# Optimization experiments

Hardware: AMD Instinct MI355X
Metric: run time of the kernel (lower is better)

Reference implementation:

```python
import jax, jax.numpy as jnp
import numpy as np

N, E, E3, DIM = 25000, 50000, 40000, 64


def setup_inputs() -> dict:
    key = jax.random.key(0)
    ks = jax.random.split(key, 16)
    def g(k, shape, scale=0.1):
        return jax.random.normal(k, shape, jnp.float32) * scale
    return {
        "x": jax.random.normal(ks[0], (N, 8), jnp.float32),
        "edge_attr": jax.random.uniform(ks[1], (E, 19), dtype=jnp.float32),
        "edge_attr3": jax.random.uniform(ks[2], (E3, 8), dtype=jnp.float32),
        "edge_index": jax.random.randint(ks[3], (2, E), 0, N),
        "edge_index3": jax.random.randint(ks[4], (2, E3), 0, N),
        "W_node": g(ks[5], (8, DIM)), "b_node": jnp.zeros((DIM,), jnp.float32),
        "W_ea": g(ks[6], (19, 12)), "b_ea": jnp.zeros((12,), jnp.float32),
        "W_e1": g(ks[7], (12, 128)), "b_e1": jnp.zeros((128,), jnp.float32),
        "W_e2": g(ks[8], (128, DIM * DIM), 0.01), "b_e2": jnp.zeros((DIM * DIM,), jnp.float32),
        "conv_bias": jnp.zeros((DIM,), jnp.float32),
        "W_ih": g(ks[9], (3 * DIM, DIM)), "b_ih": jnp.zeros((3 * DIM,), jnp.float32),
        "W_hh": g(ks[10], (3 * DIM, DIM)), "b_hh": jnp.zeros((3 * DIM,), jnp.float32),
        "W_l1": g(ks[11], (DIM + 8, 128)), "b_l1": jnp.zeros((128,), jnp.float32),
        "W_l2": g(ks[12], (128, 1)), "b_l2": jnp.zeros((1,), jnp.float32),
    }


def _forward(x, edge_attr, edge_attr3,
             W_node, b_node, W_ea, b_ea, W_e1, b_e1, W_e2, b_e2, conv_bias,
             W_ih, b_ih, W_hh, b_hh, W_l1, b_l1, W_l2, b_l2,
             edge_index, edge_index3):
    dim = W_node.shape[1]
    n = x.shape[0]
    out = jax.nn.relu(x @ W_node + b_node)                      # [N, dim]
    ea = jax.nn.relu(edge_attr @ W_ea + b_ea)                   # [E, 12]
    # edge MLP -> per-edge dim x dim weight matrices (same for all 3 conv calls)
    Wedge = (jax.nn.relu(ea @ W_e1 + b_e1) @ W_e2 + b_e2).reshape(-1, dim, dim)  # [E, dim, dim]
    src, dst = edge_index[0], edge_index[1]
    ones = jnp.ones((src.shape[0],), x.dtype)
    cnt = jnp.maximum(jax.ops.segment_sum(ones, dst, num_segments=n), 1.0)  # [N]
    h = out
    for _ in range(3):
        msg = jnp.einsum('ed,edf->ef', out[src], Wedge)                     # per-edge GEMV
        agg = jax.ops.segment_sum(msg, dst, num_segments=n) / cnt[:, None]  # scatter-mean
        m = jax.nn.relu(agg + conv_bias)
        # single-step GRU (PyTorch gate order: r, z, n)
        gi = m @ W_ih.T + b_ih
        gh = h @ W_hh.T + b_hh
        ir, iz, inn = jnp.split(gi, 3, axis=-1)
        hr, hz, hn = jnp.split(gh, 3, axis=-1)
        r = jax.nn.sigmoid(ir + hr)
        z = jax.nn.sigmoid(iz + hz)
        ng = jnp.tanh(inn + r * hn)
        h = (1.0 - z) * ng + z * h
        out = h
    pair = (out[edge_index3[0]] + out[edge_index3[1]]) * 0.5    # mean over the 2 endpoints
    yhat = jnp.concatenate([pair, edge_attr3], axis=1)          # [E3, dim+8]
    yhat = jax.nn.relu(yhat @ W_l1 + b_l1) @ W_l2 + b_l2        # [E3, 1]
    return yhat[:, 0]


def reference(x, edge_attr, edge_attr3, edge_index, edge_index3,
              W_node, b_node, W_ea, b_ea, W_e1, b_e1, W_e2, b_e2, conv_bias,
              W_ih, b_ih, W_hh, b_hh, W_l1, b_l1, W_l2, b_l2):
    return _forward(x, edge_attr, edge_attr3,
                    W_node, b_node, W_ea, b_ea, W_e1, b_e1, W_e2, b_e2, conv_bias,
                    W_ih, b_ih, W_hh, b_hh, W_l1, b_l1, W_l2, b_l2,
                    edge_index, edge_index3)
```

## Files before the change

kernel.cpp:

```cpp
#include <hip/hip_runtime.h>

typedef unsigned short u16;
typedef unsigned int u32;
typedef __attribute__((ext_vector_type(8))) short short8v;
typedef __attribute__((ext_vector_type(4))) float float4v;

__device__ __forceinline__ float sigm(float x) { return 1.0f / (1.0f + __expf(-x)); }
__device__ __forceinline__ u16 f2bf(float f) {
  u32 u = __float_as_uint(f);
  u32 r = (u + 0x7fffu + ((u >> 16) & 1u)) >> 16;
  return (u16)r;
}
__device__ __forceinline__ float bf2f(u16 w) { return __uint_as_float(((u32)w) << 16); }

__global__ void k_zero_f(float* __restrict__ p, int n) {
  int i = blockIdx.x * blockDim.x + threadIdx.x;
  if (i < n) p[i] = 0.0f;
}
__global__ void k_zero_i(int* __restrict__ p, int n) {
  int i = blockIdx.x * blockDim.x + threadIdx.x;
  if (i < n) p[i] = 0;
}

__global__ void k_cnt(const int* __restrict__ dst, int* __restrict__ cnt, int E) {
  int e = blockIdx.x * blockDim.x + threadIdx.x;
  if (e < E) atomicAdd(&cnt[dst[e]], 1);
}

__global__ void k_node(const float* __restrict__ x, const float* __restrict__ Wn,
                       const float* __restrict__ bn, float* __restrict__ h, int N) {
  int tid = blockIdx.x * blockDim.x + threadIdx.x;
  if (tid >= N * 64) return;
  int n = tid >> 6, f = tid & 63;
  float acc = bn[f];
  for (int k = 0; k < 8; ++k) acc += x[(size_t)n * 8 + k] * Wn[k * 64 + f];
  h[tid] = fmaxf(acc, 0.0f);
}

__global__ __launch_bounds__(256) void k_edge_mlp(
    const float* __restrict__ ea_in, const float* __restrict__ Wea,
    const float* __restrict__ bea, const float* __restrict__ We1,
    const float* __restrict__ be1, u16* __restrict__ Ahi, int E) {
  __shared__ float att[2][19];
  __shared__ float ea[2][12];
  int half = threadIdx.x >> 7;
  int t = threadIdx.x & 127;
  int e = blockIdx.x * 2 + half;
  bool real = (e < E);
  int ee = real ? e : E - 1;
  if (t < 19) att[half][t] = ea_in[(size_t)ee * 19 + t];
  __syncthreads();
  if (t < 12) {
    float a = bea[t];
#pragma unroll
    for (int k = 0; k < 19; ++k) a += att[half][k] * Wea[k * 12 + t];
    ea[half][t] = fmaxf(a, 0.0f);
  }
  __syncthreads();
  float a = be1[t];
#pragma unroll
  for (int j = 0; j < 12; ++j) a += ea[half][j] * We1[j * 128 + t];
  if (real) Ahi[(size_t)e * 128 + t] = f2bf(fmaxf(a, 0.0f));
}

__global__ void k_pack_b(const float* __restrict__ W2, u16* __restrict__ Bph) {
  int tid = blockIdx.x * blockDim.x + threadIdx.x;
  if (tid >= 128 * 4096) return;
  int j = tid & 7;
  int lane = (tid >> 3) & 63;
  int nt = (tid >> 9) & 3;
  int ks = (tid >> 11) & 3;
  int d = tid >> 13;
  int c = lane & 15, q = lane >> 4;
  int k = ks * 32 + q * 8 + j;
  int n = d * 64 + nt * 16 + c;
  Bph[tid] = f2bf(W2[(size_t)k * 4096 + n]);
}

__global__ void k_prep_wtf(const float* __restrict__ Wih, const float* __restrict__ Whh,
                           u16* __restrict__ WpI, u16* __restrict__ WpH) {
  int tid = blockIdx.x * blockDim.x + threadIdx.x;
  if (tid >= 2 * 12288) return;
  int w = tid / 12288;
  int r = tid - w * 12288;
  int jj = r & 7;
  int lane = (r >> 3) & 63;
  int t = r >> 9;
  int nt = t % 12, ks = t / 12;
  int c = lane & 15, q = lane >> 4;
  int j = nt * 16 + c;
  int k = ks * 32 + q * 8 + jj;
  const float* W = w ? Whh : Wih;
  u16* Wp = w ? WpH : WpI;
  Wp[r] = f2bf(W[j * 64 + k]);
}

__global__ void k_prep_wl1(const float* __restrict__ Wl1, u16* __restrict__ Wp1) {
  int tid = blockIdx.x * blockDim.x + threadIdx.x;
  if (tid >= 3 * 8 * 64 * 8) return;
  int j = tid & 7;
  int lane = (tid >> 3) & 63;
  int nt = (tid >> 9) & 7;
  int ks = tid >> 12;
  int c = lane & 15, q = lane >> 4;
  int k = ks * 32 + q * 8 + j;
  int n = nt * 16 + c;
  Wp1[tid] = f2bf((k < 72) ? Wl1[k * 128 + n] : 0.0f);
}

__global__ __launch_bounds__(256, 2) void k_conv_fused(
    const u16* __restrict__ Ahi, const u16* __restrict__ Bph,
    const float* __restrict__ b2, const float* __restrict__ h,
    const int* __restrict__ src, const int* __restrict__ dst,
    float* __restrict__ agg, int E) {
  __shared__ __align__(16) u16 sAh[128 * 136];
  __shared__ __align__(16) float hs[128 * 36];
  __shared__ __align__(16) float sb2[2048];
  int m0 = blockIdx.x * 128;
  int d0 = blockIdx.y * 32;
  int tid = threadIdx.x;
#pragma unroll
  for (int p = 0; p < 8; ++p) {
    int slot = p * 256 + tid;
    int r = slot >> 4, s = slot & 15;
    int gr = m0 + r;
    if (gr >= E) gr = E - 1;
    *(uint4*)(&sAh[r * 136 + s * 8]) = *(const uint4*)(Ahi + (size_t)gr * 128 + s * 8);
  }
#pragma unroll
  for (int p = 0; p < 4; ++p) {
    int slot = p * 256 + tid;
    int r = slot >> 3, s = slot & 7;
    int ge = m0 + r;
    if (ge >= E) ge = E - 1;
    int sn = src[ge];
    *(float4*)(&hs[r * 36 + s * 4]) = *(const float4*)(h + (size_t)sn * 64 + d0 + s * 4);
  }
#pragma unroll
  for (int p = 0; p < 2; ++p) {
    int slot = p * 256 + tid;
    *(float4*)(&sb2[slot * 4]) = *(const float4*)(b2 + d0 * 64 + slot * 4);
  }
  __syncthreads();
  int wave = tid >> 6, lane = tid & 63;
  int c = lane & 15, q = lane >> 4;
  float msg[2][4][4];
#pragma unroll
  for (int mt = 0; mt < 2; ++mt)
#pragma unroll
    for (int nt = 0; nt < 4; ++nt)
#pragma unroll
      for (int r = 0; r < 4; ++r) msg[mt][nt][r] = 0.0f;

  short8v bufA[16], bufB[16];
  auto loadB = [&](int dd, short8v* buf) {
    const u16* bp = Bph + (size_t)dd * 8192 + lane * 8;
#pragma unroll
    for (int i = 0; i < 16; ++i) buf[i] = *(const short8v*)(bp + i * 512);
  };
  auto compute = [&](int dd, const short8v* buf) {
    int dl = dd - d0;
#pragma unroll
    for (int mt = 0; mt < 2; ++mt) {
      int arow = wave * 32 + mt * 16 + c;
      float4v acc[4];
#pragma unroll
      for (int nt = 0; nt < 4; ++nt) acc[nt] = (float4v){0.f, 0.f, 0.f, 0.f};
#pragma unroll
      for (int ks = 0; ks < 4; ++ks) {
        short8v ah = *(const short8v*)(&sAh[arow * 136 + ks * 32 + q * 8]);
#pragma unroll
        for (int nt = 0; nt < 4; ++nt)
          acc[nt] = __builtin_amdgcn_mfma_f32_16x16x32_bf16(ah, buf[ks * 4 + nt], acc[nt], 0, 0, 0);
      }
      float hd[4];
#pragma unroll
      for (int r = 0; r < 4; ++r)
        hd[r] = hs[(wave * 32 + mt * 16 + q * 4 + r) * 36 + dl];
#pragma unroll
      for (int nt = 0; nt < 4; ++nt) {
        float b2v = sb2[dl * 64 + nt * 16 + c];
#pragma unroll
        for (int r = 0; r < 4; ++r) msg[mt][nt][r] += hd[r] * (acc[nt][r] + b2v);
      }
    }
  };

  loadB(d0, bufA);
  for (int d = d0; d < d0 + 32; d += 2) {
    loadB(d + 1, bufB);
    compute(d, bufA);
    if (d + 2 < d0 + 32) loadB(d + 2, bufA);
    compute(d + 1, bufB);
  }
#pragma unroll
  for (int mt = 0; mt < 2; ++mt) {
#pragma unroll
    for (int r = 0; r < 4; ++r) {
      int e = m0 + wave * 32 + mt * 16 + q * 4 + r;
      if (e < E) {
        int dn = dst[e];
        float* ap = agg + (size_t)dn * 64 + c;
#pragma unroll
        for (int nt = 0; nt < 4; ++nt) atomicAdd(ap + nt * 16, msg[mt][nt][r]);
      }
    }
  }
}

__global__ __launch_bounds__(256, 2) void k_gru_mfma(
    float* __restrict__ agg, const int* __restrict__ cnt,
    const float* __restrict__ cb, const u16* __restrict__ WpI,
    const u16* __restrict__ WpH, const float* __restrict__ bih,
    const float* __restrict__ bhh, const float* __restrict__ hin,
    float* __restrict__ hout, int N) {
  __shared__ __align__(16) u16 sM[64 * 72];
  __shared__ __align__(16) u16 sH[64 * 72];
  __shared__ __align__(16) float sHf[64 * 68];
  int n0 = blockIdx.x * 64;
  int tid = threadIdx.x;
#pragma unroll
  for (int p = 0; p < 16; ++p) {
    int slot = p * 256 + tid;
    int n = slot >> 6, f = slot & 63;
    int gn = n0 + n;
    bool real = (gn < N);
    if (!real) gn = N - 1;
    float cf = fmaxf((float)cnt[gn], 1.0f);
    float av = agg[(size_t)gn * 64 + f];
    if (real) agg[(size_t)gn * 64 + f] = 0.0f;
    float m = fmaxf(av / cf + cb[f], 0.0f);
    float hv = hin[(size_t)gn * 64 + f];
    sM[n * 72 + f] = f2bf(m);
    sH[n * 72 + f] = f2bf(hv);
    sHf[n * 68 + f] = hv;
  }
  __syncthreads();
  int wave = tid >> 6, lane = tid & 63;
  int c = lane & 15, q = lane >> 4;
  short8v am[2], ah[2];
#pragma unroll
  for (int ks = 0; ks < 2; ++ks) {
    am[ks] = *(const short8v*)(&sM[(wave * 16 + c) * 72 + ks * 32 + q * 8]);
    ah[ks] = *(const short8v*)(&sH[(wave * 16 + c) * 72 + ks * 32 + q * 8]);
  }
  float4v accRZ[8], accN[4], accHN[4];
#pragma unroll
  for (int i = 0; i < 8; ++i) accRZ[i] = (float4v){0.f, 0.f, 0.f, 0.f};
#pragma unroll
  for (int i = 0; i < 4; ++i) {
    accN[i] = (float4v){0.f, 0.f, 0.f, 0.f};
    accHN[i] = (float4v){0.f, 0.f, 0.f, 0.f};
  }
#pragma unroll
  for (int ks = 0; ks < 2; ++ks) {
#pragma unroll
    for (int nt = 0; nt < 8; ++nt) {
      short8v bI = *(const short8v*)(WpI + ((size_t)(ks * 12 + nt) * 64 + lane) * 8);
      short8v bH = *(const short8v*)(WpH + ((size_t)(ks * 12 + nt) * 64 + lane) * 8);
      accRZ[nt] = __builtin_amdgcn_mfma_f32_16x16x32_bf16(am[ks], bI, accRZ[nt], 0, 0, 0);
      accRZ[nt] = __builtin_amdgcn_mfma_f32_16x16x32_bf16(ah[ks], bH, accRZ[nt], 0, 0, 0);
    }
#pragma unroll
    for (int nt = 0; nt < 4; ++nt) {
      short8v bI = *(const short8v*)(WpI + ((size_t)(ks * 12 + 8 + nt) * 64 + lane) * 8);
      short8v bH = *(const short8v*)(WpH + ((size_t)(ks * 12 + 8 + nt) * 64 + lane) * 8);
      accN[nt] = __builtin_amdgcn_mfma_f32_16x16x32_bf16(am[ks], bI, accN[nt], 0, 0, 0);
      accHN[nt] = __builtin_amdgcn_mfma_f32_16x16x32_bf16(ah[ks], bH, accHN[nt], 0, 0, 0);
    }
  }
#pragma unroll
  for (int nt = 0; nt < 4; ++nt) {
    int f = nt * 16 + c;
    float brz_r = bih[f] + bhh[f];
    float brz_z = bih[64 + f] + bhh[64 + f];
    float bin = bih[128 + f];
    float bhn = bhh[128 + f];
#pragma unroll
    for (int r = 0; r < 4; ++r) {
      int nl = wave * 16 + q * 4 + r;
      int gn = n0 + nl;
      float rr = sigm(accRZ[nt][r] + brz_r);
      float zz = sigm(accRZ[nt + 4][r] + brz_z);
      float ng = tanhf(accN[nt][r] + bin + rr * (accHN[nt][r] + bhn));
      float hv = sHf[nl * 68 + f];
      if (gn < N) hout[(size_t)gn * 64 + f] = (1.0f - zz) * ng + zz * hv;
    }
  }
}

__global__ __launch_bounds__(256) void k_final_mfma(
    const float* __restrict__ h, const float* __restrict__ ea3,
    const int* __restrict__ idx3, const u16* __restrict__ Wp1,
    const float* __restrict__ bl1, const float* __restrict__ Wl2,
    const float* __restrict__ bl2, float* __restrict__ out, int E3) {
  __shared__ __align__(16) u16 sF[64 * 104];
  int e0 = blockIdx.x * 64;
  int tid = threadIdx.x;
  {
    int er = tid >> 2;
    int part = tid & 3;
    int ge = e0 + er;
    int gc = (ge < E3) ? ge : E3 - 1;
    int a = idx3[gc], b = idx3[E3 + gc];
    for (int kk = part * 24; kk < part * 24 + 24; ++kk) {
      float v;
      if (kk < 64) v = 0.5f * (h[(size_t)a * 64 + kk] + h[(size_t)b * 64 + kk]);
      else if (kk < 72) v = ea3[(size_t)gc * 8 + (kk - 64)];
      else v = 0.0f;
      sF[er * 104 + kk] = f2bf(v);
    }
  }
  __syncthreads();
  int wave = tid >> 6, lane = tid & 63;
  int c = lane & 15, q = lane >> 4;
  float4v acc[8];
#pragma unroll
  for (int nt = 0; nt < 8; ++nt) acc[nt] = (float4v){0.f, 0.f, 0.f, 0.f};
#pragma unroll
  for (int ks = 0; ks < 3; ++ks) {
    short8v af = *(const short8v*)(&sF[(wave * 16 + c) * 104 + ks * 32 + q * 8]);
#pragma unroll
    for (int nt = 0; nt < 8; ++nt) {
      short8v bf = *(const short8v*)(Wp1 + ((size_t)(ks * 8 + nt) * 64 + lane) * 8);
      acc[nt] = __builtin_amdgcn_mfma_f32_16x16x32_bf16(af, bf, acc[nt], 0, 0, 0);
    }
  }
  float v[4] = {0.f, 0.f, 0.f, 0.f};
#pragma unroll
  for (int nt = 0; nt < 8; ++nt) {
    int n = nt * 16 + c;
    float b1 = bl1[n];
    float w2 = Wl2[n];
#pragma unroll
    for (int r = 0; r < 4; ++r) v[r] += fmaxf(acc[nt][r] + b1, 0.0f) * w2;
  }
#pragma unroll
  for (int off = 1; off < 16; off <<= 1) {
#pragma unroll
    for (int r = 0; r < 4; ++r) v[r] += __shfl_xor(v[r], off);
  }
  if (c == 0) {
    float b2v = bl2[0];
#pragma unroll
    for (int r = 0; r < 4; ++r) {
      int e = e0 + wave * 16 + q * 4 + r;
      if (e < E3) out[e] = v[r] + b2v;
    }
  }
}

extern "C" void kernel_launch(void* const* d_in, const int* in_sizes, int n_in,
                              void* d_out, int out_size, void* d_ws, size_t ws_size,
                              hipStream_t stream) {
  const float* x          = (const float*)d_in[0];
  const float* edge_attr  = (const float*)d_in[1];
  const float* edge_attr3 = (const float*)d_in[2];
  const int*   edge_index = (const int*)d_in[3];
  const int*   edge_index3= (const int*)d_in[4];
  const float* W_node = (const float*)d_in[5];
  const float* b_node = (const float*)d_in[6];
  const float* W_ea   = (const float*)d_in[7];
  const float* b_ea   = (const float*)d_in[8];
  const float* W_e1   = (const float*)d_in[9];
  const float* b_e1   = (const float*)d_in[10];
  const float* W_e2   = (const float*)d_in[11];
  const float* b_e2   = (const float*)d_in[12];
  const float* conv_bias = (const float*)d_in[13];
  const float* W_ih   = (const float*)d_in[14];
  const float* b_ih   = (const float*)d_in[15];
  const float* W_hh   = (const float*)d_in[16];
  const float* b_hh   = (const float*)d_in[17];
  const float* W_l1   = (const float*)d_in[18];
  const float* b_l1   = (const float*)d_in[19];
  const float* W_l2   = (const float*)d_in[20];
  const float* b_l2   = (const float*)d_in[21];

  int N  = in_sizes[0] / 8;
  int E  = in_sizes[1] / 19;
  int E3 = in_sizes[2] / 8;

  char* p = (char*)d_ws;
  auto carve = [&](size_t bytes) -> void* {
    char* q = p;
    p += (bytes + 255) & ~(size_t)255;
    return (void*)q;
  };
  float* hA   = (float*)carve((size_t)N * 64 * 4);
  float* hB   = (float*)carve((size_t)N * 64 * 4);
  float* agg  = (float*)carve((size_t)N * 64 * 4);
  int*   cnt  = (int*)carve((size_t)N * 4);
  u16*   Ahi  = (u16*)carve((size_t)E * 128 * 2);
  u16*   Bph  = (u16*)carve((size_t)128 * 4096 * 2);
  u16*   WpI  = (u16*)carve(12288 * 2);
  u16*   WpH  = (u16*)carve(12288 * 2);
  u16*   Wp1  = (u16*)carve(12288 * 2);

  const int* src = edge_index;
  const int* dst = edge_index + E;

  k_zero_i<<<(N + 255) / 256, 256, 0, stream>>>(cnt, N);
  k_cnt<<<(E + 255) / 256, 256, 0, stream>>>(dst, cnt, E);
  k_node<<<((size_t)N * 64 + 255) / 256, 256, 0, stream>>>(x, W_node, b_node, hA, N);
  k_edge_mlp<<<(E + 1) / 2, 256, 0, stream>>>(edge_attr, W_ea, b_ea, W_e1, b_e1, Ahi, E);
  k_pack_b<<<(128 * 4096 + 255) / 256, 256, 0, stream>>>(W_e2, Bph);
  k_prep_wtf<<<(2 * 12288 + 255) / 256, 256, 0, stream>>>(W_ih, W_hh, WpI, WpH);
  k_prep_wl1<<<(12288 + 255) / 256, 256, 0, stream>>>(W_l1, Wp1);
  k_zero_f<<<((size_t)N * 64 + 255) / 256, 256, 0, stream>>>(agg, N * 64);

  float* hcur = hA;
  float* hnxt = hB;
  dim3 gconv((E + 127) / 128, 2);
  int ngru = (N + 63) / 64;
  for (int it = 0; it < 3; ++it) {
    k_conv_fused<<<gconv, 256, 0, stream>>>(Ahi, Bph, b_e2, hcur, src, dst, agg, E);
    k_gru_mfma<<<ngru, 256, 0, stream>>>(agg, cnt, conv_bias, WpI, WpH,
                                         b_ih, b_hh, hcur, hnxt, N);
    float* tmp = hcur; hcur = hnxt; hnxt = tmp;
  }
  k_final_mfma<<<(E3 + 63) / 64, 256, 0, stream>>>(hcur, edge_attr3, edge_index3, Wp1,
                                                   b_l1, W_l2, b_l2, (float*)d_out, E3);
}
```

Before: 448.7 us.

## Stage edge-MLP weights in LDS via async loads and keep A fragments in registers

```diff
diff --git a/kernel.cpp b/kernel.cpp
--- a/kernel.cpp
+++ b/kernel.cpp
@@ -113,20 +113,38 @@
     const float* __restrict__ b2, const float* __restrict__ h,
     const int* __restrict__ src, const int* __restrict__ dst,
     float* __restrict__ agg, int E) {
-  __shared__ __align__(16) u16 sAh[128 * 136];
+  __shared__ __align__(16) u16 sB[2][8192];
   __shared__ __align__(16) float hs[128 * 36];
   __shared__ __align__(16) float sb2[2048];
   int m0 = blockIdx.x * 128;
   int d0 = blockIdx.y * 32;
   int tid = threadIdx.x;
-#pragma unroll
-  for (int p = 0; p < 8; ++p) {
-    int slot = p * 256 + tid;
-    int r = slot >> 4, s = slot & 15;
-    int gr = m0 + r;
+  int wave = tid >> 6, lane = tid & 63;
+  int mw = wave >> 1, fw = wave & 1;
+  int c = lane & 15, q = lane >> 4;
+
+  auto stageB = [&](int d, int b) {
+    const u16* gp = Bph + (size_t)d * 8192 + wave * 2048 + lane * 8;
+    u16* lp = &sB[b][wave * 2048];
+#pragma unroll
+    for (int i = 0; i < 4; ++i)
+      __builtin_amdgcn_global_load_lds(
+          (const __attribute__((address_space(1))) unsigned int*)(gp + i * 512),
+          (__attribute__((address_space(3))) unsigned int*)(lp + i * 512), 16, 0, 0);
+  };
+
+  stageB(d0, 0);
+
+  short8v afr[4][4];
+#pragma unroll
+  for (int mt = 0; mt < 4; ++mt) {
+    int gr = m0 + mw * 64 + mt * 16 + c;
     if (gr >= E) gr = E - 1;
-    *(uint4*)(&sAh[r * 136 + s * 8]) = *(const uint4*)(Ahi + (size_t)gr * 128 + s * 8);
-  }
+    const u16* ap = Ahi + (size_t)gr * 128 + q * 8;
+#pragma unroll
+    for (int ks = 0; ks < 4; ++ks) afr[mt][ks] = *(const short8v*)(ap + ks * 32);
+  }
+
 #pragma unroll
   for (int p = 0; p < 4; ++p) {
     int slot = p * 256 + tid;
@@ -142,67 +160,60 @@
     *(float4*)(&sb2[slot * 4]) = *(const float4*)(b2 + d0 * 64 + slot * 4);
   }
   __syncthreads();
-  int wave = tid >> 6, lane = tid & 63;
-  int c = lane & 15, q = lane >> 4;
-  float msg[2][4][4];
-#pragma unroll
-  for (int mt = 0; mt < 2; ++mt)
-#pragma unroll
-    for (int nt = 0; nt < 4; ++nt)
+
+  float msg[4][2][4];
+#pragma unroll
+  for (int mt = 0; mt < 4; ++mt)
+#pragma unroll
+    for (int nt = 0; nt < 2; ++nt)
 #pragma unroll
       for (int r = 0; r < 4; ++r) msg[mt][nt][r] = 0.0f;
 
-  short8v bufA[16], bufB[16];
-  auto loadB = [&](int dd, short8v* buf) {
-    const u16* bp = Bph + (size_t)dd * 8192 + lane * 8;
-#pragma unroll
-    for (int i = 0; i < 16; ++i) buf[i] = *(const short8v*)(bp + i * 512);
-  };
-  auto compute = [&](int dd, const short8v* buf) {
-    int dl = dd - d0;
-#pragma unroll
-    for (int mt = 0; mt < 2; ++mt) {
-      int arow = wave * 32 + mt * 16 + c;
-      float4v acc[4];
-#pragma unroll
-      for (int nt = 0; nt < 4; ++nt) acc[nt] = (float4v){0.f, 0.f, 0.f, 0.f};
-#pragma unroll
-      for (int ks = 0; ks < 4; ++ks) {
-        short8v ah = *(const short8v*)(&sAh[arow * 136 + ks * 32 + q * 8]);
-#pragma unroll
-        for (int nt = 0; nt < 4; ++nt)
-          acc[nt] = __builtin_amdgcn_mfma_f32_16x16x32_bf16(ah, buf[ks * 4 + nt], acc[nt], 0, 0, 0);
+  int cur = 0;
+  for (int dl = 0; dl < 32; ++dl) {
+    if (dl < 31) stageB(d0 + dl + 1, cur ^ 1);
+    float4v acc[4][2];
+#pragma unroll
+    for (int mt = 0; mt < 4; ++mt)
+#pragma unroll
+      for (int nt = 0; nt < 2; ++nt) acc[mt][nt] = (float4v){0.f, 0.f, 0.f, 0.f};
+#pragma unroll
+    for (int ks = 0; ks < 4; ++ks) {
+      short8v b0 = *(const short8v*)(&sB[cur][ks * 2048 + fw * 1024 + lane * 8]);
+      short8v b1 = *(const short8v*)(&sB[cur][ks * 2048 + fw * 1024 + 512 + lane * 8]);
+#pragma unroll
+      for (int mt = 0; mt < 4; ++mt) {
+        acc[mt][0] = __builtin_amdgcn_mfma_f32_16x16x32_bf16(afr[mt][ks], b0, acc[mt][0], 0, 0, 0);
+        acc[mt][1] = __builtin_amdgcn_mfma_f32_16x16x32_bf16(afr[mt][ks], b1, acc[mt][1], 0, 0, 0);
       }
+    }
+#pragma unroll
+    for (int mt = 0; mt < 4; ++mt) {
       float hd[4];
 #pragma unroll
       for (int r = 0; r < 4; ++r)
-        hd[r] = hs[(wave * 32 + mt * 16 + q * 4 + r) * 36 + dl];
-#pragma unroll
-      for (int nt = 0; nt < 4; ++nt) {
-        float b2v = sb2[dl * 64 + nt * 16 + c];
-#pragma unroll
-        for (int r = 0; r < 4; ++r) msg[mt][nt][r] += hd[r] * (acc[nt][r] + b2v);
+        hd[r] = hs[(mw * 64 + mt * 16 + q * 4 + r) * 36 + dl];
+#pragma unroll
+      for (int nt = 0; nt < 2; ++nt) {
+        float b2v = sb2[dl * 64 + fw * 32 + nt * 16 + c];
+#pragma unroll
+        for (int r = 0; r < 4; ++r) msg[mt][nt][r] += hd[r] * (acc[mt][nt][r] + b2v);
       }
     }
-  };
-
-  loadB(d0, bufA);
-  for (int d = d0; d < d0 + 32; d += 2) {
-    loadB(d + 1, bufB);
-    compute(d, bufA);
-    if (d + 2 < d0 + 32) loadB(d + 2, bufA);
-    compute(d + 1, bufB);
-  }
-#pragma unroll
-  for (int mt = 0; mt < 2; ++mt) {
+    __syncthreads();
+    cur ^= 1;
+  }
+
+#pragma unroll
+  for (int mt = 0; mt < 4; ++mt) {
 #pragma unroll
     for (int r = 0; r < 4; ++r) {
-      int e = m0 + wave * 32 + mt * 16 + q * 4 + r;
+      int e = m0 + mw * 64 + mt * 16 + q * 4 + r;
       if (e < E) {
         int dn = dst[e];
-        float* ap = agg + (size_t)dn * 64 + c;
-#pragma unroll
-        for (int nt = 0; nt < 4; ++nt) atomicAdd(ap + nt * 16, msg[mt][nt][r]);
+        float* ap = agg + (size_t)dn * 64 + fw * 32 + c;
+#pragma unroll
+        for (int nt = 0; nt < 2; ++nt) atomicAdd(ap + nt * 16, msg[mt][nt][r]);
       }
     }
   }
```

Result: slower. 466.1 us (+3.9%).
